# Performance work log

Hardware: AMD Instinct MI355X
Metric: run time of the kernel (lower is better)

The kernel has to match this reference:

```python
import jax, jax.numpy as jnp
import numpy as np
import math

D = 768
H = 12
HD = D // H  # 64
DFF = 4 * D


def _layernorm(x, g, b, eps=1e-5):
    mu = jnp.mean(x, axis=-1, keepdims=True)
    var = jnp.var(x, axis=-1, keepdims=True)
    return (x - mu) * jax.lax.rsqrt(var + eps) * g + b


def _new_gelu(x):
    c = math.sqrt(2.0 / math.pi)
    return 0.5 * x * (1.0 + jnp.tanh(c * (x + 0.044715 * x * x * x)))


def setup_inputs() -> dict:
    key = jax.random.key(0)
    ks = jax.random.split(key, 8)
    B, N = 8, 1024
    s = 0.02
    return {
        "x": jax.random.normal(ks[0], (B, N, D), jnp.float32),
        "pad_mask": jnp.ones((B, N), jnp.int32),
        "ln1_g": jnp.ones((D,), jnp.float32),
        "ln1_b": jnp.zeros((D,), jnp.float32),
        "w_attn": jax.random.normal(ks[1], (D, 3 * D), jnp.float32) * s,
        "b_attn": jnp.zeros((3 * D,), jnp.float32),
        "w_proj": jax.random.normal(ks[2], (D, D), jnp.float32) * s,
        "b_proj": jnp.zeros((D,), jnp.float32),
        "ln2_g": jnp.ones((D,), jnp.float32),
        "ln2_b": jnp.zeros((D,), jnp.float32),
        "w_fc": jax.random.normal(ks[3], (D, DFF), jnp.float32) * s,
        "b_fc": jnp.zeros((DFF,), jnp.float32),
        "w_fc2": jax.random.normal(ks[4], (DFF, D), jnp.float32) * s,
        "b_fc2": jnp.zeros((D,), jnp.float32),
    }


def reference(x, pad_mask, ln1_g, ln1_b, w_attn, b_attn, w_proj, b_proj,
              ln2_g, ln2_b, w_fc, b_fc, w_fc2, b_fc2):
    B, N, C = x.shape
    # --- attention branch (note: source's causal masked_fill is NOT in-place,
    # so the causal mask is effectively never applied; only pad_mask is) ---
    h = _layernorm(x, ln1_g, ln1_b)
    qkv = h @ w_attn + b_attn  # [B,N,3D]
    q, k, v = jnp.split(qkv, 3, axis=-1)
    q = q.reshape(B, N, H, HD).transpose(0, 2, 1, 3)  # [B,H,N,hd]
    k = k.reshape(B, N, H, HD).transpose(0, 2, 1, 3)
    v = v.reshape(B, N, H, HD).transpose(0, 2, 1, 3)
    att = jnp.einsum('bhqd,bhkd->bhqk', q, k) * (1.0 / math.sqrt(HD))
    # pad mask broadcasts as [B,1,N,1]: masks query rows where pad==0
    att = jnp.where(pad_mask[:, None, :, None] == 0, -jnp.inf, att)
    att = jax.nn.softmax(att, axis=-1)
    o = jnp.einsum('bhqk,bhkd->bhqd', att, v)
    o = o.transpose(0, 2, 1, 3).reshape(B, N, C)
    x = x + (o @ w_proj + b_proj)
    # --- MLP branch ---
    h2 = _layernorm(x, ln2_g, ln2_b)
    x = x + (_new_gelu(h2 @ w_fc + b_fc) @ w_fc2 + b_fc2)
    return x
```

## Files before the change

### kernel.cpp

```cpp
#include <hip/hip_runtime.h>
#include <hip/hip_bf16.h>

typedef __bf16 bf16;
typedef __bf16 bf16x8 __attribute__((ext_vector_type(8)));
typedef __bf16 bf16x4 __attribute__((ext_vector_type(4)));
typedef float f32x4 __attribute__((ext_vector_type(4)));

#define SEQ 1024
#define BATCH 8
#define DM 768
#define NH 12
#define HDIM 64
#define DFF 3072
#define NTOK (BATCH*SEQ)

#define AS1 __attribute__((address_space(1)))
#define AS3 __attribute__((address_space(3)))
#define MFMA16(a, b, c) __builtin_amdgcn_mfma_f32_16x16x32_bf16(a, b, c, 0, 0, 0)

__device__ __forceinline__ float gelu_f(float x) {
  const float c = 0.7978845608028654f;
  float z = c * (x + 0.044715f * x * x * x);
  return x / (1.0f + __expf(-2.0f * z));
}

__global__ __launch_bounds__(256) void transpose4_kernel(
    const float* __restrict__ in0, bf16* __restrict__ out0,
    const float* __restrict__ in1, bf16* __restrict__ out1,
    const float* __restrict__ in2, bf16* __restrict__ out2,
    const float* __restrict__ in3, bf16* __restrict__ out3) {
  __shared__ float tile[32][33];
  int id = blockIdx.x;
  const float* in; bf16* out; int R, C;
  if (id < 1728)      { in = in0; out = out0; R = 768;  C = 2304; }
  else if (id < 2304) { in = in1; out = out1; R = 768;  C = 768;  id -= 1728; }
  else if (id < 4608) { in = in2; out = out2; R = 768;  C = 3072; id -= 2304; }
  else                { in = in3; out = out3; R = 3072; C = 768;  id -= 4608; }
  int nc = C >> 5;
  int c0 = (id % nc) * 32, r0 = (id / nc) * 32;
  int tx = threadIdx.x & 31, ty = threadIdx.x >> 5;
  #pragma unroll
  for (int i = 0; i < 4; ++i)
    tile[ty + i * 8][tx] = in[(size_t)(r0 + ty + i * 8) * C + c0 + tx];
  __syncthreads();
  #pragma unroll
  for (int i = 0; i < 4; ++i)
    out[(size_t)(c0 + ty + i * 8) * R + r0 + tx] = (bf16)tile[tx][ty + i * 8];
}

__global__ __launch_bounds__(256) void ln_kernel(
    const float* __restrict__ x, const float* __restrict__ g,
    const float* __restrict__ bta, bf16* __restrict__ out) {
  int row = blockIdx.x;
  int tid = threadIdx.x;
  const float* xr = x + (size_t)row * DM;
  float v0 = xr[tid], v1 = xr[tid + 256], v2 = xr[tid + 512];
  float s1 = v0 + v1 + v2;
  float s2 = v0 * v0 + v1 * v1 + v2 * v2;
  #pragma unroll
  for (int m = 32; m >= 1; m >>= 1) {
    s1 += __shfl_xor(s1, m, 64);
    s2 += __shfl_xor(s2, m, 64);
  }
  __shared__ float ps1[4], ps2[4];
  int wid = tid >> 6;
  if ((tid & 63) == 0) { ps1[wid] = s1; ps2[wid] = s2; }
  __syncthreads();
  float t1 = ps1[0] + ps1[1] + ps1[2] + ps1[3];
  float t2 = ps2[0] + ps2[1] + ps2[2] + ps2[3];
  float mean = t1 * (1.0f / DM);
  float var = t2 * (1.0f / DM) - mean * mean;
  float rstd = rsqrtf(var + 1e-5f);
  bf16* orow = out + (size_t)row * DM;
  orow[tid]       = (bf16)((v0 - mean) * rstd * g[tid]       + bta[tid]);
  orow[tid + 256] = (bf16)((v1 - mean) * rstd * g[tid + 256] + bta[tid + 256]);
  orow[tid + 512] = (bf16)((v2 - mean) * rstd * g[tid + 512] + bta[tid + 512]);
}

__global__ __launch_bounds__(256) void reduce_ln_kernel(
    const float* __restrict__ p0, const float* __restrict__ p1,
    const float* __restrict__ bias, const float* __restrict__ resid,
    const float* __restrict__ g, const float* __restrict__ bta,
    bf16* __restrict__ x1b, bf16* __restrict__ h) {
  int row = blockIdx.x;
  int tid = threadIdx.x;
  size_t base = (size_t)row * DM;
  float v0 = p0[base + tid]       + p1[base + tid]       + bias[tid]       + resid[base + tid];
  float v1 = p0[base + tid + 256] + p1[base + tid + 256] + bias[tid + 256] + resid[base + tid + 256];
  float v2 = p0[base + tid + 512] + p1[base + tid + 512] + bias[tid + 512] + resid[base + tid + 512];
  bf16* xr = x1b + base;
  xr[tid]       = (bf16)v0;
  xr[tid + 256] = (bf16)v1;
  xr[tid + 512] = (bf16)v2;
  float s1 = v0 + v1 + v2;
  float s2 = v0 * v0 + v1 * v1 + v2 * v2;
  #pragma unroll
  for (int m = 32; m >= 1; m >>= 1) {
    s1 += __shfl_xor(s1, m, 64);
    s2 += __shfl_xor(s2, m, 64);
  }
  __shared__ float ps1[4], ps2[4];
  int wid = tid >> 6;
  if ((tid & 63) == 0) { ps1[wid] = s1; ps2[wid] = s2; }
  __syncthreads();
  float t1 = ps1[0] + ps1[1] + ps1[2] + ps1[3];
  float t2 = ps2[0] + ps2[1] + ps2[2] + ps2[3];
  float mean = t1 * (1.0f / DM);
  float var = t2 * (1.0f / DM) - mean * mean;
  float rstd = rsqrtf(var + 1e-5f);
  bf16* orow = h + base;
  orow[tid]       = (bf16)((v0 - mean) * rstd * g[tid]       + bta[tid]);
  orow[tid + 256] = (bf16)((v1 - mean) * rstd * g[tid + 256] + bta[tid + 256]);
  orow[tid + 512] = (bf16)((v2 - mean) * rstd * g[tid + 512] + bta[tid + 512]);
}

__global__ __launch_bounds__(256) void reduce_out_kernel(
    const float* __restrict__ p0, const float* __restrict__ p1,
    const float* __restrict__ bias, const bf16* __restrict__ resid,
    float* __restrict__ out) {
  int i = blockIdx.x * 256 + threadIdx.x;
  size_t e = (size_t)i * 4;
  f32x4 a = *(const f32x4*)(p0 + e);
  f32x4 b = *(const f32x4*)(p1 + e);
  f32x4 bs = *(const f32x4*)(bias + (int)(e % DM));
  bf16x4 r = *(const bf16x4*)(resid + e);
  f32x4 o;
  #pragma unroll
  for (int j = 0; j < 4; ++j) o[j] = a[j] + b[j] + bs[j] + (float)r[j];
  *(f32x4*)(out + e) = o;
}

__global__ __launch_bounds__(512, 4) void gemm_kernel(
    const bf16* __restrict__ A, int lda, const bf16* __restrict__ BT,
    const float* __restrict__ bias, const float* __restrict__ residF,
    const bf16* __restrict__ residB,
    float* __restrict__ outF, bf16* __restrict__ outB,
    int N, int K, int flags) {
  __shared__ bf16 As[3][128 * 32];
  __shared__ bf16 Bs[3][256 * 32];
  int tid = threadIdx.x;
  int wid = tid >> 6, lane = tid & 63;
  int nct = N >> 8;
  int nwg = gridDim.x;
  int bid = blockIdx.x;
  int lid = ((nwg & 7) == 0) ? ((bid & 7) * (nwg >> 3) + (bid >> 3)) : bid;
  int row0, col0, koff = 0, Keff = K;
  size_t outOff = 0;
  if (flags & 2) {
    int half = nwg >> 1;
    int s = lid / half;
    int r = lid - s * half;
    int nrt = half / nct;
    col0 = (r / nrt) << 8;
    row0 = (r % nrt) << 7;
    Keff = K >> 1;
    koff = s * Keff;
    outOff = (size_t)s * ((size_t)nrt << 7) * (size_t)N;
  } else {
    row0 = (lid / nct) * 128;
    col0 = (lid % nct) * 256;
  }
  int wm = wid >> 2, wn = wid & 3;
  int fr = lane & 15, fq = lane >> 4;
  f32x4 acc[4][4] = {};

  int srow = tid >> 2;
  int ssl = ((tid & 3) ^ ((tid >> 3) & 3)) * 8;
  const bf16* gA  = A + (size_t)(row0 + srow) * lda + koff + ssl;
  const bf16* gB  = BT + (size_t)(col0 + srow) * K + koff + ssl;
  const bf16* gB2 = gB + (size_t)128 * K;
  int ldsA  = (wid * 16) * 32;
  int ldsB  = (wid * 16) * 32;
  int ldsB2 = (128 + wid * 16) * 32;

  int RB0 = wn * 64 + 0 * 16 + fr, RB1 = wn * 64 + 1 * 16 + fr;
  int RB2 = wn * 64 + 2 * 16 + fr, RB3 = wn * 64 + 3 * 16 + fr;
  int RA0 = wm * 64 + 0 * 16 + fr, RA1 = wm * 64 + 1 * 16 + fr;
  int RA2 = wm * 64 + 2 * 16 + fr, RA3 = wm * 64 + 3 * 16 + fr;
  int offB0 = RB0 * 32 + (fq ^ ((RB0 >> 1) & 3)) * 8;
  int offB1 = RB1 * 32 + (fq ^ ((RB1 >> 1) & 3)) * 8;
  int offB2 = RB2 * 32 + (fq ^ ((RB2 >> 1) & 3)) * 8;
  int offB3 = RB3 * 32 + (fq ^ ((RB3 >> 1) & 3)) * 8;
  int offA0 = RA0 * 32 + (fq ^ ((RA0 >> 1) & 3)) * 8;
  int offA1 = RA1 * 32 + (fq ^ ((RA1 >> 1) & 3)) * 8;
  int offA2 = RA2 * 32 + (fq ^ ((RA2 >> 1) & 3)) * 8;
  int offA3 = RA3 * 32 + (fq ^ ((RA3 >> 1) & 3)) * 8;

  int nt = Keff >> 5;

  __builtin_amdgcn_global_load_lds((const AS1 void*)(gA), (AS3 void*)(&As[0][ldsA]), 16, 0, 0);
  __builtin_amdgcn_global_load_lds((const AS1 void*)(gB), (AS3 void*)(&Bs[0][ldsB]), 16, 0, 0);
  __builtin_amdgcn_global_load_lds((const AS1 void*)(gB2), (AS3 void*)(&Bs[0][ldsB2]), 16, 0, 0);
  __builtin_amdgcn_global_load_lds((const AS1 void*)(gA + 32), (AS3 void*)(&As[1][ldsA]), 16, 0, 0);
  __builtin_amdgcn_global_load_lds((const AS1 void*)(gB + 32), (AS3 void*)(&Bs[1][ldsB]), 16, 0, 0);
  __builtin_amdgcn_global_load_lds((const AS1 void*)(gB2 + 32), (AS3 void*)(&Bs[1][ldsB2]), 16, 0, 0);

#define KS(CB, T)                                                              \
  {                                                                            \
    if ((T) == nt - 1) asm volatile("s_waitcnt vmcnt(0)" ::: "memory");        \
    else               asm volatile("s_waitcnt vmcnt(3)" ::: "memory");        \
    __builtin_amdgcn_s_barrier();                                              \
    bf16x8 b0 = *(const bf16x8*)&Bs[CB][offB0];                                \
    bf16x8 b1 = *(const bf16x8*)&Bs[CB][offB1];                                \
    bf16x8 b2 = *(const bf16x8*)&Bs[CB][offB2];                                \
    bf16x8 b3 = *(const bf16x8*)&Bs[CB][offB3];                                \
    bf16x8 a0 = *(const bf16x8*)&As[CB][offA0];                                \
    bf16x8 a1 = *(const bf16x8*)&As[CB][offA1];                                \
    if ((T) + 2 < nt)                                                          \
      __builtin_amdgcn_global_load_lds(                                        \
          (const AS1 void*)(gA + ((T) + 2) * 32),                              \
          (AS3 void*)(&As[((CB) + 2) % 3][ldsA]), 16, 0, 0);                   \
    __builtin_amdgcn_s_barrier();                                              \
    __builtin_amdgcn_s_setprio(1);                                             \
    acc[0][0] = MFMA16(a0, b0, acc[0][0]); acc[0][1] = MFMA16(a0, b1, acc[0][1]); \
    acc[0][2] = MFMA16(a0, b2, acc[0][2]); acc[0][3] = MFMA16(a0, b3, acc[0][3]); \
    acc[1][0] = MFMA16(a1, b0, acc[1][0]); acc[1][1] = MFMA16(a1, b1, acc[1][1]); \
    acc[1][2] = MFMA16(a1, b2, acc[1][2]); acc[1][3] = MFMA16(a1, b3, acc[1][3]); \
    __builtin_amdgcn_s_setprio(0);                                             \
    bf16x8 a2 = *(const bf16x8*)&As[CB][offA2];                                \
    bf16x8 a3 = *(const bf16x8*)&As[CB][offA3];                                \
    if ((T) + 2 < nt) {                                                        \
      __builtin_amdgcn_global_load_lds(                                        \
          (const AS1 void*)(gB + ((T) + 2) * 32),                              \
          (AS3 void*)(&Bs[((CB) + 2) % 3][ldsB]), 16, 0, 0);                   \
      __builtin_amdgcn_global_load_lds(                                        \
          (const AS1 void*)(gB2 + ((T) + 2) * 32),                             \
          (AS3 void*)(&Bs[((CB) + 2) % 3][ldsB2]), 16, 0, 0);                  \
    }                                                                          \
    __builtin_amdgcn_s_barrier();                                              \
    __builtin_amdgcn_s_setprio(1);                                             \
    acc[2][0] = MFMA16(a2, b0, acc[2][0]); acc[2][1] = MFMA16(a2, b1, acc[2][1]); \
    acc[2][2] = MFMA16(a2, b2, acc[2][2]); acc[2][3] = MFMA16(a2, b3, acc[2][3]); \
    acc[3][0] = MFMA16(a3, b0, acc[3][0]); acc[3][1] = MFMA16(a3, b1, acc[3][1]); \
    acc[3][2] = MFMA16(a3, b2, acc[3][2]); acc[3][3] = MFMA16(a3, b3, acc[3][3]); \
    __builtin_amdgcn_s_setprio(0);                                             \
  }

  for (int t = 0; t < nt; t += 3) {
    KS(0, t);
    KS(1, t + 1);
    KS(2, t + 2);
  }
#undef KS

  bool gelu = (flags & 1);
  #pragma unroll
  for (int m = 0; m < 4; ++m) {
    #pragma unroll
    for (int n = 0; n < 4; ++n) {
      int col = col0 + wn * 64 + n * 16 + fr;
      float bs = bias ? bias[col] : 0.f;
      #pragma unroll
      for (int r = 0; r < 4; ++r) {
        int row = row0 + wm * 64 + m * 16 + fq * 4 + r;
        float v = acc[m][n][r] + bs;
        if (gelu) v = gelu_f(v);
        if (residF) v += residF[(size_t)row * N + col];
        if (residB) v += (float)residB[(size_t)row * N + col];
        if (outF) outF[outOff + (size_t)row * N + col] = v;
        else outB[(size_t)row * N + col] = (bf16)v;
      }
    }
  }
}

__global__ __launch_bounds__(256) void vtrans_kernel(
    const bf16* __restrict__ qkv, bf16* __restrict__ vt) {
  int bh = blockIdx.y;
  int b = bh / NH, h = bh % NH;
  int n0 = blockIdx.x * 64;
  __shared__ bf16 tile[64][65];
  int tx = threadIdx.x & 63, ty = threadIdx.x >> 6;
  #pragma unroll
  for (int i = 0; i < 16; ++i) {
    int n = ty + i * 4;
    tile[tx][n] = qkv[(size_t)(b * SEQ + n0 + n) * (3 * DM) + 2 * DM + h * HDIM + tx];
  }
  __syncthreads();
  #pragma unroll
  for (int i = 0; i < 16; ++i) {
    int hd = ty + i * 4;
    vt[((size_t)bh * HDIM + hd) * SEQ + n0 + tx] = tile[hd][tx];
  }
}

__global__ __launch_bounds__(256) void attn_kernel(
    bf16* __restrict__ qkv, const bf16* __restrict__ vt,
    const int* __restrict__ pad) {
  __shared__ bf16 Ks[2][64 * 64];
  __shared__ bf16 Vs[2][64 * 64];
  __shared__ bf16 P_lds[4][16 * 72];
  int blk = blockIdx.x;
  int lblk = (blk & 7) * 192 + (blk >> 3);
  int qt = lblk & 15;
  int bh = lblk >> 4;
  int b = bh / NH, h = bh % NH;
  int tid = threadIdx.x, wid = tid >> 6, lane = tid & 63;
  int q0 = qt * 64 + wid * 16;
  int fr = lane & 15;
  int fq = lane >> 4;
  int fk = fq * 8;
  const bf16* qbase = qkv + (size_t)(b * SEQ + q0) * (3 * DM) + h * HDIM;
  bf16* Pw = &P_lds[wid][0];
  bf16x8 qf[2];
  #pragma unroll
  for (int kk = 0; kk < 2; ++kk)
    qf[kk] = *(const bf16x8*)(qbase + (size_t)fr * (3 * DM) + kk * 32 + fk);
  int srow = (wid << 4) + (lane >> 3);
  int sc = ((lane & 7) << 4) ^ ((lane >> 3) << 4);
  const bf16* kSrc = qkv + (size_t)(b * SEQ + srow) * (3 * DM) + DM + h * HDIM + (sc >> 1);
  const bf16* vSrc = vt + ((size_t)bh * HDIM + srow) * SEQ + (sc >> 1);

  auto STAGE = [&](int buf, int kt) {
    const bf16* kS = kSrc + (size_t)kt * 64 * (3 * DM);
    const bf16* vS = vSrc + kt * 64;
    bf16* kD = &Ks[buf][wid * 1024];
    bf16* vD = &Vs[buf][wid * 1024];
    __builtin_amdgcn_global_load_lds((const AS1 void*)kS, (AS3 void*)kD, 16, 0, 0);
    __builtin_amdgcn_global_load_lds((const AS1 void*)(kS + 8 * (3 * DM)), (AS3 void*)(kD + 512), 16, 0, 0);
    __builtin_amdgcn_global_load_lds((const AS1 void*)vS, (AS3 void*)vD, 16, 0, 0);
    __builtin_amdgcn_global_load_lds((const AS1 void*)(vS + 8 * SEQ), (AS3 void*)(vD + 512), 16, 0, 0);
  };

  float lp[4] = {0.f, 0.f, 0.f, 0.f};
  f32x4 oacc[4] = {};
  int padv[4];
  #pragma unroll
  for (int r = 0; r < 4; ++r) padv[r] = pad[b * SEQ + q0 + fq * 4 + r];
  bool anymask = __any(padv[0] == 0 || padv[1] == 0 || padv[2] == 0 || padv[3] == 0);
  int xr = (fr & 7) << 4;

  STAGE(0, 0);
  for (int kt = 0; kt < 16; ++kt) {
    int cur = kt & 1;
    if (kt < 15) STAGE(cur ^ 1, kt + 1);
    if (kt == 15) asm volatile("s_waitcnt vmcnt(0)" ::: "memory");
    else          asm volatile("s_waitcnt vmcnt(4)" ::: "memory");
    __builtin_amdgcn_s_barrier();

    f32x4 s[4];
    #pragma unroll
    for (int nt = 0; nt < 4; ++nt) {
      f32x4 a = {};
      #pragma unroll
      for (int kk = 0; kk < 2; ++kk) {
        int colb = (kk * 64 + fq * 16) ^ xr;
        bf16x8 kf = *(const bf16x8*)&Ks[cur][(nt * 16 + fr) * 64 + (colb >> 1)];
        a = __builtin_amdgcn_mfma_f32_16x16x32_bf16(qf[kk], kf, a, 0, 0, 0);
      }
      s[nt] = a;
    }
    if (anymask) {
      #pragma unroll
      for (int r = 0; r < 4; ++r)
        if (padv[r] == 0) { s[0][r] = 0.f; s[1][r] = 0.f; s[2][r] = 0.f; s[3][r] = 0.f; }
    }
    #pragma unroll
    for (int nt = 0; nt < 4; ++nt)
      #pragma unroll
      for (int r = 0; r < 4; ++r)
        s[nt][r] = __expf(s[nt][r] * 0.125f);
    #pragma unroll
    for (int r = 0; r < 4; ++r)
      lp[r] += (s[0][r] + s[1][r]) + (s[2][r] + s[3][r]);
    #pragma unroll
    for (int nt = 0; nt < 4; ++nt)
      #pragma unroll
      for (int r = 0; r < 4; ++r)
        Pw[(fq * 4 + r) * 72 + nt * 16 + fr] = (bf16)s[nt][r];
    #pragma unroll
    for (int nt = 0; nt < 4; ++nt) {
      #pragma unroll
      for (int ks = 0; ks < 2; ++ks) {
        bf16x8 pf = *(const bf16x8*)&Pw[fr * 72 + ks * 32 + fk];
        int colb = (ks * 64 + fq * 16) ^ xr;
        bf16x8 vf = *(const bf16x8*)&Vs[cur][(nt * 16 + fr) * 64 + (colb >> 1)];
        oacc[nt] = __builtin_amdgcn_mfma_f32_16x16x32_bf16(pf, vf, oacc[nt], 0, 0, 0);
      }
    }
    __builtin_amdgcn_s_barrier();
  }
  #pragma unroll
  for (int r = 0; r < 4; ++r) {
    float l = lp[r];
    #pragma unroll
    for (int msk = 8; msk >= 1; msk >>= 1) l += __shfl_xor(l, msk, 64);
    float inv = 1.0f / l;
    #pragma unroll
    for (int nt = 0; nt < 4; ++nt)
      qkv[(size_t)(b * SEQ + q0 + fq * 4 + r) * (3 * DM) + h * HDIM + nt * 16 + fr] =
          (bf16)(oacc[nt][r] * inv);
  }
}

extern "C" void kernel_launch(void* const* d_in, const int* in_sizes, int n_in,
                              void* d_out, int out_size, void* d_ws, size_t ws_size,
                              hipStream_t stream) {
  const float* x      = (const float*)d_in[0];
  const int*   pad    = (const int*)d_in[1];
  const float* ln1_g  = (const float*)d_in[2];
  const float* ln1_b  = (const float*)d_in[3];
  const float* w_attn = (const float*)d_in[4];
  const float* b_attn = (const float*)d_in[5];
  const float* w_proj = (const float*)d_in[6];
  const float* b_proj = (const float*)d_in[7];
  const float* ln2_g  = (const float*)d_in[8];
  const float* ln2_b  = (const float*)d_in[9];
  const float* w_fc   = (const float*)d_in[10];
  const float* b_fc   = (const float*)d_in[11];
  const float* w_fc2  = (const float*)d_in[12];
  const float* b_fc2  = (const float*)d_in[13];
  float* out = (float*)d_out;

  char* ws = (char*)d_ws;
  size_t off = 0;
  auto alloc = [&](size_t bytes) {
    void* p = ws + off;
    off += (bytes + 255) & ~(size_t)255;
    return p;
  };
  bf16* wT_attn = (bf16*)alloc((size_t)(3 * DM) * DM * 2);
  bf16* wT_proj = (bf16*)alloc((size_t)DM * DM * 2);
  bf16* wT_fc   = (bf16*)alloc((size_t)DFF * DM * 2);
  bf16* wT_fc2  = (bf16*)alloc((size_t)DM * DFF * 2);
  bf16* h       = (bf16*)alloc((size_t)NTOK * DM * 2);
  bf16* qkv     = (bf16*)alloc((size_t)NTOK * (3 * DM) * 2);
  bf16* vt      = (bf16*)alloc((size_t)BATCH * NH * HDIM * SEQ * 2);
  bf16* x1b     = (bf16*)alloc((size_t)NTOK * DM * 2);
  bf16* act     = (bf16*)alloc((size_t)NTOK * DFF * 2);

  float* partP = (float*)act;
  float* partF = (float*)h;

  transpose4_kernel<<<6912, 256, 0, stream>>>(
      w_attn, wT_attn, w_proj, wT_proj, w_fc, wT_fc, w_fc2, wT_fc2);
  ln_kernel<<<NTOK, 256, 0, stream>>>(x, ln1_g, ln1_b, h);
  gemm_kernel<<<576, 512, 0, stream>>>(
      h, DM, wT_attn, b_attn, nullptr, nullptr, nullptr, qkv, 3 * DM, DM, 0);
  vtrans_kernel<<<dim3(SEQ / 64, BATCH * NH), 256, 0, stream>>>(qkv, vt);
  attn_kernel<<<BATCH * NH * (SEQ / 64), 256, 0, stream>>>(qkv, vt, pad);
  gemm_kernel<<<384, 512, 0, stream>>>(
      qkv, 3 * DM, wT_proj, nullptr, nullptr, nullptr, partP, nullptr, DM, DM, 2);
  reduce_ln_kernel<<<NTOK, 256, 0, stream>>>(
      partP, partP + (size_t)NTOK * DM, b_proj, x, ln2_g, ln2_b, x1b, h);
  gemm_kernel<<<768, 512, 0, stream>>>(
      h, DM, wT_fc, b_fc, nullptr, nullptr, nullptr, act, DFF, DM, 1);
  gemm_kernel<<<384, 512, 0, stream>>>(
      act, DFF, wT_fc2, nullptr, nullptr, nullptr, partF, nullptr, DM, DFF, 2);
  reduce_out_kernel<<<(NTOK * DM) / (4 * 256), 256, 0, stream>>>(
      partF, partF + (size_t)NTOK * DM, b_fc2, x1b, out);
}
```

Baseline: 290.9 us.

## Add 256x256 eight-phase GEMM kernel for MLP layers and drop mid-tile barriers

Adds a new GEMM kernel with 256x256 output tiles, 64-wide K slabs, double-buffered LDS with XOR swizzle, and an eight-phase schedule that interleaves global-to-LDS loads with MFMA bursts. The two MLP GEMMs (fc and fc2 split-K) use it, which halves the workgroup count and raises operand reuse per LDS load. Separately, two s_barrier calls are removed from the existing gemm_kernel's inner step. The new kernel uses 128KB LDS and more accumulators, which lowers occupancy, and removing the barriers risks races on LDS buffer reuse.

New measurement: 312.8 us. +7.5%, slower.

```diff
diff --git a/kernel.cpp b/kernel.cpp
--- a/kernel.cpp
+++ b/kernel.cpp
@@ -128,6 +128,168 @@
   #pragma unroll
   for (int j = 0; j < 4; ++j) o[j] = a[j] + b[j] + bs[j] + (float)r[j];
   *(f32x4*)(out + e) = o;
+}
+
+__global__ __launch_bounds__(512, 2) void gemm8p_kernel(
+    const bf16* __restrict__ A, int lda, const bf16* __restrict__ BT,
+    const float* __restrict__ bias, const float* __restrict__ residF,
+    const bf16* __restrict__ residB,
+    float* __restrict__ outF, bf16* __restrict__ outB,
+    int N, int K, int flags) {
+  __shared__ bf16 As[2][256 * 64];
+  __shared__ bf16 Bs[2][256 * 64];
+  int tid = threadIdx.x;
+  int wid = tid >> 6, lane = tid & 63;
+  int nct = N >> 8;
+  int nwg = gridDim.x;
+  int bid = blockIdx.x;
+  int lid = (bid & 7) * (nwg >> 3) + (bid >> 3);
+  int row0, col0, koff = 0, Keff = K;
+  size_t outOff = 0;
+  if (flags & 2) {
+    int half = nwg >> 1;
+    int s = lid / half;
+    int r = lid - s * half;
+    int nrt = half / nct;
+    col0 = (r / nrt) << 8;
+    row0 = (r % nrt) << 8;
+    Keff = K >> 1;
+    koff = s * Keff;
+    outOff = (size_t)s * ((size_t)nrt << 8) * (size_t)N;
+  } else {
+    int nrt = nwg / nct;
+    col0 = (lid / nrt) << 8;
+    row0 = (lid % nrt) << 8;
+  }
+  int wm = wid >> 2, wn = wid & 3;
+  int fr = lane & 15, fq = lane >> 4;
+  f32x4 acc[8][4] = {};
+
+  int srow = tid >> 3;
+  int ssl = ((tid & 7) ^ ((tid >> 3) & 7)) * 8;
+  const bf16* gA = A + (size_t)(row0 + srow) * lda + koff + ssl;
+  const bf16* gB = BT + (size_t)(col0 + srow) * K + koff + ssl;
+  int ldsw = wid * 512;
+
+  int aoff0 = (wm * 128 + fr) * 64 + ((0 * 4 + fq) ^ (fr & 7)) * 8;
+  int aoff1 = (wm * 128 + fr) * 64 + ((1 * 4 + fq) ^ (fr & 7)) * 8;
+  int boff0 = (wn * 64 + fr) * 64 + ((0 * 4 + fq) ^ (fr & 7)) * 8;
+  int boff1 = (wn * 64 + fr) * 64 + ((1 * 4 + fq) ^ (fr & 7)) * 8;
+
+  int nt = Keff >> 6;
+
+#define SA(BUF, SLAB, KT)                                                      \
+  __builtin_amdgcn_global_load_lds(                                            \
+      (const AS1 void*)(gA + (size_t)(SLAB) * 64 * lda + (KT) * 64),           \
+      (AS3 void*)(&As[BUF][(SLAB) * 4096 + ldsw]), 16, 0, 0)
+#define SB(BUF, SLAB, KT)                                                      \
+  __builtin_amdgcn_global_load_lds(                                            \
+      (const AS1 void*)(gB + (size_t)(SLAB) * 64 * K + (KT) * 64),             \
+      (AS3 void*)(&Bs[BUF][(SLAB) * 4096 + ldsw]), 16, 0, 0)
+
+  SA(0, 0, 0); SA(0, 2, 0);
+  SB(0, 0, 0); SB(0, 1, 0); SB(0, 2, 0); SB(0, 3, 0);
+  SA(0, 1, 0); SA(0, 3, 0);
+
+#define TILE(CB, T)                                                            \
+  {                                                                            \
+    bf16x8 bb0[4], bb1[4], aa[4];                                              \
+                                                \
+    asm volatile("s_waitcnt vmcnt(2)" ::: "memory");                           \
+    __builtin_amdgcn_s_barrier();                                              \
+    __builtin_amdgcn_sched_barrier(0);                                         \
+    _Pragma("unroll")                                                          \
+    for (int n = 0; n < 4; ++n) bb0[n] = *(const bf16x8*)&Bs[CB][boff0 + n * 1024]; \
+    _Pragma("unroll")                                                          \
+    for (int m = 0; m < 4; ++m) aa[m] = *(const bf16x8*)&As[CB][aoff0 + m * 1024]; \
+    if ((T) + 1 < nt) { SA((CB) ^ 1, 0, (T) + 1); SA((CB) ^ 1, 2, (T) + 1); }  \
+    asm volatile("s_waitcnt lgkmcnt(0)" ::: "memory");                         \
+    __builtin_amdgcn_sched_barrier(0);                                         \
+    __builtin_amdgcn_s_barrier();                                              \
+    __builtin_amdgcn_s_setprio(1);                                             \
+    _Pragma("unroll")                                                          \
+    for (int m = 0; m < 4; ++m)                                                \
+      _Pragma("unroll")                                                        \
+      for (int n = 0; n < 4; ++n) acc[m][n] = MFMA16(aa[m], bb0[n], acc[m][n]);\
+    __builtin_amdgcn_s_setprio(0);                                             \
+                                                \
+    if ((T) + 1 < nt) asm volatile("s_waitcnt vmcnt(2)" ::: "memory");         \
+    else              asm volatile("s_waitcnt vmcnt(0)" ::: "memory");         \
+    __builtin_amdgcn_s_barrier();                                              \
+    __builtin_amdgcn_sched_barrier(0);                                         \
+    _Pragma("unroll")                                                          \
+    for (int m = 0; m < 4; ++m) aa[m] = *(const bf16x8*)&As[CB][aoff0 + (4 + m) * 1024]; \
+    _Pragma("unroll")                                                          \
+    for (int n = 0; n < 4; ++n) bb1[n] = *(const bf16x8*)&Bs[CB][boff1 + n * 1024]; \
+    if ((T) + 1 < nt) { SB((CB) ^ 1, 0, (T) + 1); SB((CB) ^ 1, 1, (T) + 1); }  \
+    asm volatile("s_waitcnt lgkmcnt(0)" ::: "memory");                         \
+    __builtin_amdgcn_sched_barrier(0);                                         \
+    __builtin_amdgcn_s_barrier();                                              \
+    __builtin_amdgcn_s_setprio(1);                                             \
+    _Pragma("unroll")                                                          \
+    for (int m = 0; m < 4; ++m)                                                \
+      _Pragma("unroll")                                                        \
+      for (int n = 0; n < 4; ++n) acc[4 + m][n] = MFMA16(aa[m], bb0[n], acc[4 + m][n]); \
+    __builtin_amdgcn_s_setprio(0);                                             \
+                                                \
+    __builtin_amdgcn_s_barrier();                                              \
+    __builtin_amdgcn_sched_barrier(0);                                         \
+    _Pragma("unroll")                                                          \
+    for (int m = 0; m < 4; ++m) aa[m] = *(const bf16x8*)&As[CB][aoff1 + m * 1024]; \
+    if ((T) + 1 < nt) { SB((CB) ^ 1, 2, (T) + 1); SB((CB) ^ 1, 3, (T) + 1); }  \
+    asm volatile("s_waitcnt lgkmcnt(0)" ::: "memory");                         \
+    __builtin_amdgcn_sched_barrier(0);                                         \
+    __builtin_amdgcn_s_barrier();                                              \
+    __builtin_amdgcn_s_setprio(1);                                             \
+    _Pragma("unroll")                                                          \
+    for (int m = 0; m < 4; ++m)                                                \
+      _Pragma("unroll")                                                        \
+      for (int n = 0; n < 4; ++n) acc[m][n] = MFMA16(aa[m], bb1[n], acc[m][n]);\
+    __builtin_amdgcn_s_setprio(0);                                             \
+                                                \
+    __builtin_amdgcn_s_barrier();                                              \
+    __builtin_amdgcn_sched_barrier(0);                                         \
+    _Pragma("unroll")                                                          \
+    for (int m = 0; m < 4; ++m) aa[m] = *(const bf16x8*)&As[CB][aoff1 + (4 + m) * 1024]; \
+    if ((T) + 1 < nt) { SA((CB) ^ 1, 1, (T) + 1); SA((CB) ^ 1, 3, (T) + 1); }  \
+    asm volatile("s_waitcnt lgkmcnt(0)" ::: "memory");                         \
+    __builtin_amdgcn_sched_barrier(0);                                         \
+    __builtin_amdgcn_s_barrier();                                              \
+    __builtin_amdgcn_s_setprio(1);                                             \
+    _Pragma("unroll")                                                          \
+    for (int m = 0; m < 4; ++m)                                                \
+      _Pragma("unroll")                                                        \
+      for (int n = 0; n < 4; ++n) acc[4 + m][n] = MFMA16(aa[m], bb1[n], acc[4 + m][n]); \
+    __builtin_amdgcn_s_setprio(0);                                             \
+  }
+
+  for (int t = 0; t < nt; t += 2) {
+    TILE(0, t);
+    TILE(1, t + 1);
+  }
+#undef TILE
+#undef SA
+#undef SB
+
+  bool gelu = (flags & 1);
+  #pragma unroll
+  for (int m = 0; m < 8; ++m) {
+    #pragma unroll
+    for (int n = 0; n < 4; ++n) {
+      int col = col0 + wn * 64 + n * 16 + fr;
+      float bs = bias ? bias[col] : 0.f;
+      #pragma unroll
+      for (int r = 0; r < 4; ++r) {
+        int row = row0 + wm * 128 + m * 16 + fq * 4 + r;
+        float v = acc[m][n][r] + bs;
+        if (gelu) v = gelu_f(v);
+        if (residF) v += residF[(size_t)row * N + col];
+        if (residB) v += (float)residB[(size_t)row * N + col];
+        if (outF) outF[outOff + (size_t)row * N + col] = v;
+        else outB[(size_t)row * N + col] = (bf16)v;
+      }
+    }
+  }
 }
 
 __global__ __launch_bounds__(512, 4) void gemm_kernel(
@@ -210,7 +372,6 @@
       __builtin_amdgcn_global_load_lds(                                        \
           (const AS1 void*)(gA + ((T) + 2) * 32),                              \
           (AS3 void*)(&As[((CB) + 2) % 3][ldsA]), 16, 0, 0);                   \
-    __builtin_amdgcn_s_barrier();                                              \
     __builtin_amdgcn_s_setprio(1);                                             \
     acc[0][0] = MFMA16(a0, b0, acc[0][0]); acc[0][1] = MFMA16(a0, b1, acc[0][1]); \
     acc[0][2] = MFMA16(a0, b2, acc[0][2]); acc[0][3] = MFMA16(a0, b3, acc[0][3]); \
@@ -227,7 +388,6 @@
           (const AS1 void*)(gB2 + ((T) + 2) * 32),                             \
           (AS3 void*)(&Bs[((CB) + 2) % 3][ldsB2]), 16, 0, 0);                  \
     }                                                                          \
-    __builtin_amdgcn_s_barrier();                                              \
     __builtin_amdgcn_s_setprio(1);                                             \
     acc[2][0] = MFMA16(a2, b0, acc[2][0]); acc[2][1] = MFMA16(a2, b1, acc[2][1]); \
     acc[2][2] = MFMA16(a2, b2, acc[2][2]); acc[2][3] = MFMA16(a2, b3, acc[2][3]); \
@@ -443,9 +603,9 @@
       qkv, 3 * DM, wT_proj, nullptr, nullptr, nullptr, partP, nullptr, DM, DM, 2);
   reduce_ln_kernel<<<NTOK, 256, 0, stream>>>(
       partP, partP + (size_t)NTOK * DM, b_proj, x, ln2_g, ln2_b, x1b, h);
-  gemm_kernel<<<768, 512, 0, stream>>>(
+  gemm8p_kernel<<<384, 512, 0, stream>>>(
       h, DM, wT_fc, b_fc, nullptr, nullptr, nullptr, act, DFF, DM, 1);
-  gemm_kernel<<<384, 512, 0, stream>>>(
+  gemm8p_kernel<<<192, 512, 0, stream>>>(
       act, DFF, wT_fc2, nullptr, nullptr, nullptr, partF, nullptr, DM, DFF, 2);
   reduce_out_kernel<<<(NTOK * DM) / (4 * 256), 256, 0, stream>>>(
       partF, partF + (size_t)NTOK * DM, b_fc2, x1b, out);
```
